# Kernel tuning notes

Hardware: AMD Instinct MI355X
Metric: run time of the kernel (lower is better)

## Reference

```python
import jax, jax.numpy as jnp
import numpy as np
from jax import lax

B = 512
THRESHOLD = 0.5
CFG = [64, 64, 'M', 128, 128, 'M', 256, 256, 256, 'M', 512, 512, 512, 'M', 512, 512, 512, 'M']  # VGG16


def _conv_relu(x, w, b):
    # x: [B,C,H,W], w: [O,I,3,3] (torch OIHW layout), pad=1 stride=1
    y = lax.conv_general_dilated(x, w, (1, 1), 'SAME',
                                 dimension_numbers=('NCHW', 'OIHW', 'NCHW'))
    return jax.nn.relu(y + b[None, :, None, None])


def _maxpool2(x):
    return lax.reduce_window(x, -jnp.inf, lax.max, (1, 1, 2, 2), (1, 1, 2, 2), 'VALID')


def _features(x, ws, bs):
    i = 0
    for c in CFG:
        if c == 'M':
            x = _maxpool2(x)
        else:
            x = _conv_relu(x, ws[i], bs[i])
            i += 1
    return x  # [B,512,1,1]


def _gcn(distance):
    # Faithful translation, including the source bug: 'onetensor' is zeros_like,
    # so mask==0 everywhere and A_hat collapses to the identity.
    n = distance.shape[0]
    zero = jnp.zeros_like(distance)
    one = jnp.zeros_like(distance)  # bug in original: torch.zeros_like for onetensor
    adj = jnp.where(distance > THRESHOLD, distance, zero)
    mask = jnp.where(distance > THRESHOLD, one, zero)
    idx = lax.top_k(adj, 10)[1]                                   # [n,10]
    top10 = jnp.zeros_like(adj).at[jnp.arange(n)[:, None], idx].set(1.0)
    top10 = top10 * mask
    a_hat = top10 + jnp.eye(n, dtype=distance.dtype)
    d_inv = jnp.diag(1.0 / jnp.sum(a_hat, axis=1))
    return lax.stop_gradient(a_hat @ d_inv)                        # [n,n]


def _forward(x, target, conv_ws, conv_bs, lin1_w, lin1_b, lin2_w, lin2_b, cls_w, cls_b):
    feat = _features(x, conv_ws, conv_bs).reshape(x.shape[0], -1)  # [B,512]
    h = jax.nn.relu(feat @ lin1_w + lin1_b)                        # [B,256]
    low = h @ lin2_w + lin2_b                                      # [B,128]
    graph_pre = jax.nn.sigmoid(low @ low.T)                        # [B,B]
    graph_gt = (target[:, None] == target[None, :]).astype(jnp.float32)
    mat = _gcn(graph_pre)                                          # [B,B], detached
    out = (mat @ feat) @ cls_w + cls_b                             # [B,10]
    return out, graph_pre, graph_gt


def setup_inputs() -> dict:
    key = jax.random.key(0)
    ks = iter(jax.random.split(key, 64))
    inp = {}
    inp['x'] = jax.random.normal(next(ks), (B, 3, 32, 32), dtype=jnp.float32)
    inp['target'] = jax.random.randint(next(ks), (B,), 0, 10)
    in_c, i = 3, 0
    for c in CFG:
        if c == 'M':
            continue
        scale = 1.0 / np.sqrt(in_c * 9.0)
        inp['conv%d_w' % i] = jax.random.normal(next(ks), (c, in_c, 3, 3), dtype=jnp.float32) * scale
        inp['conv%d_b' % i] = jnp.zeros((c,), dtype=jnp.float32)
        in_c, i = c, i + 1
    inp['lin1_w'] = jax.random.normal(next(ks), (512, 256), dtype=jnp.float32) * (1.0 / np.sqrt(512.0))
    inp['lin1_b'] = jnp.zeros((256,), dtype=jnp.float32)
    inp['lin2_w'] = jax.random.normal(next(ks), (256, 128), dtype=jnp.float32) * (1.0 / np.sqrt(256.0))
    inp['lin2_b'] = jnp.zeros((128,), dtype=jnp.float32)
    inp['cls_w'] = jax.random.normal(next(ks), (512, 10), dtype=jnp.float32) * (1.0 / np.sqrt(512.0))
    inp['cls_b'] = jnp.zeros((10,), dtype=jnp.float32)
    return inp


def reference(x, target,
              conv0_w, conv0_b, conv1_w, conv1_b, conv2_w, conv2_b, conv3_w, conv3_b,
              conv4_w, conv4_b, conv5_w, conv5_b, conv6_w, conv6_b, conv7_w, conv7_b,
              conv8_w, conv8_b, conv9_w, conv9_b, conv10_w, conv10_b, conv11_w, conv11_b,
              conv12_w, conv12_b,
              lin1_w, lin1_b, lin2_w, lin2_b, cls_w, cls_b):
    ws = [conv0_w, conv1_w, conv2_w, conv3_w, conv4_w, conv5_w, conv6_w,
          conv7_w, conv8_w, conv9_w, conv10_w, conv11_w, conv12_w]
    bs = [conv0_b, conv1_b, conv2_b, conv3_b, conv4_b, conv5_b, conv6_b,
          conv7_b, conv8_b, conv9_b, conv10_b, conv11_b, conv12_b]
    return _forward(x, target, ws, bs, lin1_w, lin1_b, lin2_w, lin2_b, cls_w, cls_b)
```

## Files before the change

kernel.cpp:

```cpp
#include <hip/hip_runtime.h>

typedef unsigned short u16;
typedef __bf16 bf16x8 __attribute__((ext_vector_type(8)));
typedef float floatx4 __attribute__((ext_vector_type(4)));

__device__ inline u16 f2bf(float f) {
    return __builtin_bit_cast(u16, (__bf16)f);
}
__device__ inline float bf2f(u16 h) {
    return __uint_as_float(((unsigned int)h) << 16);
}

__device__ __forceinline__ void async_copy16(u16* lds, const u16* g) {
    __builtin_amdgcn_global_load_lds(
        (const __attribute__((address_space(1))) unsigned int*)(uintptr_t)g,
        (__attribute__((address_space(3))) unsigned int*)(unsigned int)(uintptr_t)lds,
        16, 0, 0);
}

__global__ void zero_halo(u16* __restrict__ buf, int Hp, int C, int total8)
{
    int i = blockIdx.x * 256 + threadIdx.x;
    if (i >= total8) return;
    int c8 = i % (C / 8);
    int p  = i / (C / 8);
    int ring = 4 * Hp - 4;
    int h = p % ring;
    int b = p / ring;
    int y, x;
    if (h < Hp)              { y = 0;              x = h; }
    else if (h < 2 * Hp)     { y = Hp - 1;         x = h - Hp; }
    else if (h < 3 * Hp - 2) { y = h - 2 * Hp + 1; x = 0; }
    else                     { y = h - 3 * Hp + 3; x = Hp - 1; }
    uint4 z = make_uint4(0u, 0u, 0u, 0u);
    *(uint4*)(buf + ((size_t)((b * Hp + y) * Hp + x) * C) + c8 * 8) = z;
}

__global__ __launch_bounds__(256) void conv0_kernel(
    const float* __restrict__ x, const float* __restrict__ w,
    const float* __restrict__ bias, u16* __restrict__ out)
{
    __shared__ __align__(16) float xs[3][6][36];
    const int t  = threadIdx.x;
    const int b  = blockIdx.x >> 3;
    const int y0 = (blockIdx.x & 7) * 4;

    for (int i = t; i < 3 * 6 * 36; i += 256) {
        int ci  = i / 216;
        int rem = i % 216;
        int r   = rem / 36;
        int c   = rem % 36;
        int gy  = y0 - 1 + r;
        int gx  = c - 1;
        float v = 0.f;
        if ((unsigned)gy < 32u && (unsigned)gx < 32u)
            v = x[((b * 3 + ci) * 32 + gy) * 32 + gx];
        xs[ci][r][c] = v;
    }
    const int lane = t & 63;
    const int wv   = t >> 6;
    float wr[27];
    #pragma unroll
    for (int k = 0; k < 27; k++) wr[k] = w[lane * 27 + k];
    const float bz = bias[lane];
    __syncthreads();

    const int y = y0 + wv;
    u16* orow = out + ((size_t)((b * 34 + y + 1) * 34 + 1) * 64) + lane;
    for (int xg = 0; xg < 32; xg += 4) {
        float a0 = bz, a1 = bz, a2 = bz, a3 = bz;
        #pragma unroll
        for (int ci = 0; ci < 3; ci++) {
            #pragma unroll
            for (int rr = 0; rr < 3; rr++) {
                const float* row = &xs[ci][wv + rr][0];
                float4 c03 = *(const float4*)(row + xg);
                float2 c45 = *(const float2*)(row + xg + 4);
                float w0 = wr[ci * 9 + rr * 3 + 0];
                float w1 = wr[ci * 9 + rr * 3 + 1];
                float w2 = wr[ci * 9 + rr * 3 + 2];
                a0 += c03.x * w0 + c03.y * w1 + c03.z * w2;
                a1 += c03.y * w0 + c03.z * w1 + c03.w * w2;
                a2 += c03.z * w0 + c03.w * w1 + c45.x * w2;
                a3 += c03.w * w0 + c45.x * w1 + c45.y * w2;
            }
        }
        orow[(xg + 0) * 64] = f2bf(fmaxf(a0, 0.f));
        orow[(xg + 1) * 64] = f2bf(fmaxf(a1, 0.f));
        orow[(xg + 2) * 64] = f2bf(fmaxf(a2, 0.f));
        orow[(xg + 3) * 64] = f2bf(fmaxf(a3, 0.f));
    }
}

struct RepackArgs {
    const float* src[14];
    u16* dst[14];
    int p1[14];
    int p2[14];
    int startBlk[15];
    int nseg;
};

__global__ __launch_bounds__(256) void repack_all(RepackArgs a)
{
    __shared__ __align__(16) u16 lds[9216];
    int blk = blockIdx.x;
    int s = 0;
    #pragma unroll 1
    while (s + 1 < a.nseg && blk >= a.startBlk[s + 1]) s++;
    const int cb = blk - a.startBlk[s];
    const int t  = threadIdx.x;

    if (a.p2[s] == 0) {
        const int Cin = a.p1[s];
        const int logCin = __builtin_ctz(Cin);
        const float* src = a.src[s] + (size_t)cb * 9216;
        u16* dst = a.dst[s] + (size_t)cb * 9216;
        #pragma unroll
        for (int it = 0; it < 9; it++) {
            int j4 = it * 256 + t;
            float4 v = *(const float4*)(src + j4 * 4);
            ushort4 h;
            h.x = f2bf(v.x); h.y = f2bf(v.y); h.z = f2bf(v.z); h.w = f2bf(v.w);
            *(ushort4*)(lds + j4 * 4) = h;
        }
        __syncthreads();
        #pragma unroll
        for (int it = 0; it < 9; it++) {
            int o4   = (it * 256 + t) * 4;
            int ci   = o4 & (Cin - 1);
            int rest = o4 >> logCin;
            int co   = rest / 9;
            int sh   = rest - co * 9;
            int sb   = (co << logCin) * 9 + ci * 9 + sh;
            ushort4 h;
            h.x = lds[sb]; h.y = lds[sb + 9]; h.z = lds[sb + 18]; h.w = lds[sb + 27];
            *(ushort4*)(dst + o4) = h;
        }
    } else {
        const int K = a.p1[s], N = a.p2[s];
        const int ntx = N >> 6;
        const int k0 = (cb / ntx) * 64, n0 = (cb % ntx) * 64;
        const float* src = a.src[s];
        u16* dst = a.dst[s];
        const int r = t >> 4, c4 = (t & 15) * 4;
        #pragma unroll
        for (int rr = 0; rr < 64; rr += 16) {
            float4 v = *(const float4*)(src + (size_t)(k0 + r + rr) * N + n0 + c4);
            u16* p = lds + (r + rr) * 72 + c4;
            p[0] = f2bf(v.x); p[1] = f2bf(v.y); p[2] = f2bf(v.z); p[3] = f2bf(v.w);
        }
        __syncthreads();
        #pragma unroll
        for (int it = 0; it < 2; it++) {
            int ov = it * 256 + t;
            int n  = ov >> 3;
            int kq = (ov & 7) * 8;
            __align__(16) u16 h[8];
            #pragma unroll
            for (int j = 0; j < 8; j++) h[j] = lds[(kq + j) * 72 + n];
            *(uint4*)(dst + (size_t)(n0 + n) * K + k0 + kq) = *(uint4*)h;
        }
    }
}

template <int BM, int BN>
__global__ __launch_bounds__(256) void conv_gemm(
    const u16* __restrict__ in, const u16* __restrict__ wt,
    const float* __restrict__ bias, u16* __restrict__ out,
    float* __restrict__ partial, size_t pstride,
    int H, int Cin, int Cout, int logHW, int logW, int splitN,
    int outPad, int poolMode)
{
    constexpr int BK = 64;
    constexpr int WC = (BM == 256) ? BN : (BN / 2);
    constexpr int NT = WC / 16;
    constexpr int NB_A = BM / 32;
    constexpr int NB_B = BN / 32;
    __shared__ u16 As[BM * BK];
    __shared__ u16 Bs[BN * BK];

    const int Nblocks = Cout / BN;
    const int per = gridDim.x >> 3;
    const int bid = (blockIdx.x & 7) * per + (blockIdx.x >> 3);
    const int sp   = bid % splitN;
    const int tile = bid / splitN;
    const int m0 = (tile / Nblocks) * BM;
    const int n0 = (tile % Nblocks) * BN;

    const int t    = threadIdx.x;
    const int lane = t & 63;
    const int wave = t >> 6;
    const int quad = lane >> 4;
    const int l16  = lane & 15;
    const int wm   = (BM == 256) ? wave : (wave >> 1);
    const int wn   = (BM == 256) ? 0 : (wave & 1);
    const int W    = H;
    const int Wp   = H + 2;
    const int HW   = 1 << logHW;
    const int col8 = t & 7;
    const int r0   = t >> 3;
    const int scol = col8 ^ (r0 & 7);

    const int CinB = Cin * 2;

    int vA[NB_A];
    #pragma unroll
    for (int j = 0; j < NB_A; j++) {
        int m  = m0 + r0 + 32 * j;
        int b  = m >> logHW;
        int rm = m & (HW - 1);
        int y  = rm >> logW;
        int xx = rm & (W - 1);
        vA[j] = ((b * Wp + y + 1) * Wp + xx + 1) * CinB + scol * 16;
    }
    int vB[NB_B];
    #pragma unroll
    for (int j = 0; j < NB_B; j++)
        vB[j] = (n0 + r0 + 32 * j) * 9 * CinB + scol * 16;

    const int logKB = (Cin == 64) ? 0 : (Cin == 128) ? 1 : (Cin == 256) ? 2 : 3;
    const int KB  = 1 << logKB;
    const int T   = 9 * KB;
    const int len = T / splitN;
    const int it0 = sp * len;

    int s0 = it0 >> logKB;
    int c3 = s0 - (s0 / 3) * 3;
    int ta = ((s0 / 3 - 1) * Wp + (c3 - 1)) * CinB;
    int kb = (it0 & (KB - 1)) * 128;
    int tb = it0 * 128;

    u16* const ldsA = As + t * 8;
    u16* const ldsB = Bs + t * 8;
    const char* const inB = (const char*)in;
    const char* const wtB = (const char*)wt;

    floatx4 acc[4][NT];
    #pragma unroll
    for (int i = 0; i < 4; i++)
        #pragma unroll
        for (int j = 0; j < NT; j++)
            acc[i][j] = (floatx4){0.f, 0.f, 0.f, 0.f};

    const int sw = (l16 & 7) * 8;

    for (int it = 0; it < len; it++) {
        const int ua = ta + kb;
        #pragma unroll
        for (int j = 0; j < NB_A; j++)
            async_copy16(ldsA + j * 2048, (const u16*)(inB + (ua + vA[j])));
        #pragma unroll
        for (int j = 0; j < NB_B; j++)
            async_copy16(ldsB + j * 2048, (const u16*)(wtB + (tb + vB[j])));
        __syncthreads();
        #pragma unroll
        for (int kk = 0; kk < BK; kk += 32) {
            bf16x8 af[4], bfv[NT];
            int cbo = kk + quad * 8;
            #pragma unroll
            for (int mt = 0; mt < 4; mt++)
                af[mt] = *(const bf16x8*)(As + (wm * 64 + mt * 16 + l16) * 64 + (cbo ^ sw));
            #pragma unroll
            for (int nt = 0; nt < NT; nt++)
                bfv[nt] = *(const bf16x8*)(Bs + (wn * WC + nt * 16 + l16) * 64 + (cbo ^ sw));
            #pragma unroll
            for (int mt = 0; mt < 4; mt++)
                #pragma unroll
                for (int nt = 0; nt < NT; nt++)
                    acc[mt][nt] = __builtin_amdgcn_mfma_f32_16x16x32_bf16(
                        af[mt], bfv[nt], acc[mt][nt], 0, 0, 0);
        }
        __syncthreads();
        tb += 128;
        kb += 128;
        if (kb == CinB) {
            kb = 0;
            ta += (c3 == 2) ? (Wp - 2) * CinB : CinB;
            c3 = (c3 == 2) ? 0 : c3 + 1;
        }
    }

    const int ngb = n0 + wn * WC + l16;

    if (splitN > 1) {
        float* pout = partial + (size_t)sp * pstride;
        #pragma unroll
        for (int mt = 0; mt < 4; mt++)
            #pragma unroll
            for (int r = 0; r < 4; r++) {
                int mg = m0 + wm * 64 + mt * 16 + quad * 4 + r;
                float* op = pout + (size_t)mg * Cout + ngb;
                #pragma unroll
                for (int nt = 0; nt < NT; nt++)
                    op[nt * 16] = acc[mt][nt][r];
            }
        return;
    }

    float bzv[NT];
    #pragma unroll
    for (int nt = 0; nt < NT; nt++) bzv[nt] = bias[ngb + nt * 16];

    if (poolMode) {
        const int Hpo = (H >> 1) + 2;
        if (logW == 5) {
            #pragma unroll
            for (int mt = 0; mt < 2; mt++)
                #pragma unroll
                for (int rp = 0; rp < 2; rp++) {
                    int m1 = m0 + wm * 64 + mt * 16 + quad * 4 + 2 * rp;
                    int b  = m1 >> logHW;
                    int rm = m1 & (HW - 1);
                    int yp = (rm >> logW) >> 1;
                    int xp = (rm & (W - 1)) >> 1;
                    u16* op = out + (size_t)((b * Hpo + yp + 1) * Hpo + xp + 1) * Cout + ngb;
                    #pragma unroll
                    for (int nt = 0; nt < NT; nt++) {
                        float v = fmaxf(
                            fmaxf(acc[mt][nt][2 * rp], acc[mt][nt][2 * rp + 1]),
                            fmaxf(acc[mt + 2][nt][2 * rp], acc[mt + 2][nt][2 * rp + 1]));
                        op[nt * 16] = f2bf(fmaxf(v + bzv[nt], 0.f));
                    }
                }
        } else if (logW == 4) {
            #pragma unroll
            for (int mtp = 0; mtp < 2; mtp++)
                #pragma unroll
                for (int rp = 0; rp < 2; rp++) {
                    int mt = 2 * mtp;
                    int m1 = m0 + wm * 64 + mt * 16 + quad * 4 + 2 * rp;
                    int b  = m1 >> logHW;
                    int rm = m1 & (HW - 1);
                    int yp = (rm >> logW) >> 1;
                    int xp = (rm & (W - 1)) >> 1;
                    u16* op = out + (size_t)((b * Hpo + yp + 1) * Hpo + xp + 1) * Cout + ngb;
                    #pragma unroll
                    for (int nt = 0; nt < NT; nt++) {
                        float v = fmaxf(
                            fmaxf(acc[mt][nt][2 * rp], acc[mt][nt][2 * rp + 1]),
                            fmaxf(acc[mt + 1][nt][2 * rp], acc[mt + 1][nt][2 * rp + 1]));
                        op[nt * 16] = f2bf(fmaxf(v + bzv[nt], 0.f));
                    }
                }
        } else {
            #pragma unroll
            for (int mt = 0; mt < 4; mt++)
                #pragma unroll
                for (int rp = 0; rp < 2; rp++) {
                    int m1 = m0 + wm * 64 + mt * 16 + quad * 4 + 2 * rp;
                    int b  = m1 >> logHW;
                    int rm = m1 & (HW - 1);
                    int yp = (rm >> logW) >> 1;
                    int xp = (rm & (W - 1)) >> 1;
                    u16* op = out + (size_t)((b * Hpo + yp + 1) * Hpo + xp + 1) * Cout + ngb;
                    #pragma unroll
                    for (int nt = 0; nt < NT; nt++) {
                        float a = fmaxf(acc[mt][nt][2 * rp], acc[mt][nt][2 * rp + 1]);
                        float p = __shfl_xor(a, 32, 64);
                        float v = fmaxf(a, p);
                        if (quad < 2)
                            op[nt * 16] = f2bf(fmaxf(v + bzv[nt], 0.f));
                    }
                }
        }
        return;
    }

    #pragma unroll
    for (int mt = 0; mt < 4; mt++) {
        #pragma unroll
        for (int r = 0; r < 4; r++) {
            int mg = m0 + wm * 64 + mt * 16 + quad * 4 + r;
            size_t obase;
            if (outPad) {
                int b  = mg >> logHW;
                int rm = mg & (HW - 1);
                int y  = rm >> logW;
                int xx = rm & (W - 1);
                obase = (size_t)((b * Wp + y + 1) * Wp + xx + 1) * Cout;
            } else {
                obase = (size_t)mg * Cout;
            }
            u16* op = out + obase + ngb;
            #pragma unroll
            for (int nt = 0; nt < NT; nt++)
                op[nt * 16] = f2bf(fmaxf(acc[mt][nt][r] + bzv[nt], 0.f));
        }
    }
}

__global__ void reduce_split(const float* __restrict__ partial,
                             const float* __restrict__ bias, u16* __restrict__ out,
                             int MN, int C, int logC, int splitN, size_t pstride,
                             int H, int logHW, int logW, int outPad)
{
    int i4 = (blockIdx.x * 256 + threadIdx.x) * 4;
    if (i4 >= MN) return;
    float4 s = *(const float4*)(partial + i4);
    for (int sp = 1; sp < splitN; sp++) {
        float4 p = *(const float4*)(partial + (size_t)sp * pstride + i4);
        s.x += p.x; s.y += p.y; s.z += p.z; s.w += p.w;
    }
    int n = i4 & (C - 1);
    int m = i4 >> logC;
    size_t obase;
    if (outPad) {
        int Wp = H + 2;
        int b  = m >> logHW;
        int rm = m & ((1 << logHW) - 1);
        int y  = rm >> logW;
        int xx = rm & (H - 1);
        obase = (size_t)((b * Wp + y + 1) * Wp + xx + 1) * C;
    } else {
        obase = (size_t)m * C;
    }
    ushort4 o;
    o.x = f2bf(fmaxf(s.x + bias[n + 0], 0.f));
    o.y = f2bf(fmaxf(s.y + bias[n + 1], 0.f));
    o.z = f2bf(fmaxf(s.z + bias[n + 2], 0.f));
    o.w = f2bf(fmaxf(s.w + bias[n + 3], 0.f));
    *(ushort4*)(out + obase + n) = o;
}

__global__ void reduce_pool(const float* __restrict__ partial,
                            const float* __restrict__ bias, u16* __restrict__ out,
                            int total4, int C, int splitN, size_t pstride,
                            int H, int outPad)
{
    int idx = blockIdx.x * 256 + threadIdx.x;
    if (idx >= total4) return;
    int c4 = idx % (C / 4);
    int p  = idx / (C / 4);
    int Ho = H >> 1;
    int xp = p % Ho; p /= Ho;
    int yp = p % Ho;
    int b  = p / Ho;
    int n  = c4 * 4;
    float4 best;
    bool first = true;
    #pragma unroll
    for (int dy = 0; dy < 2; dy++)
        #pragma unroll
        for (int dx = 0; dx < 2; dx++) {
            int m = (b * H + 2 * yp + dy) * H + 2 * xp + dx;
            const float* q = partial + (size_t)m * C + n;
            float4 s = *(const float4*)q;
            for (int sp = 1; sp < splitN; sp++) {
                float4 pp = *(const float4*)(q + (size_t)sp * pstride);
                s.x += pp.x; s.y += pp.y; s.z += pp.z; s.w += pp.w;
            }
            if (first) { best = s; first = false; }
            else {
                best.x = fmaxf(best.x, s.x); best.y = fmaxf(best.y, s.y);
                best.z = fmaxf(best.z, s.z); best.w = fmaxf(best.w, s.w);
            }
        }
    size_t obase;
    if (outPad) {
        int Hpo = Ho + 2;
        obase = (size_t)((b * Hpo + yp + 1) * Hpo + xp + 1) * C;
    } else {
        obase = (size_t)((b * Ho + yp) * Ho + xp) * C;
    }
    ushort4 o;
    o.x = f2bf(fmaxf(best.x + bias[n + 0], 0.f));
    o.y = f2bf(fmaxf(best.y + bias[n + 1], 0.f));
    o.z = f2bf(fmaxf(best.z + bias[n + 2], 0.f));
    o.w = f2bf(fmaxf(best.w + bias[n + 3], 0.f));
    *(ushort4*)(out + obase + n) = o;
}

template <bool RELU, bool OUTBF>
__global__ __launch_bounds__(256) void gemm64(
    const u16* __restrict__ A, const u16* __restrict__ Bt,
    const float* __restrict__ bias, void* __restrict__ outv,
    int M, int N, int K)
{
    constexpr int LDP = 72;
    __shared__ u16 As[64 * LDP];
    __shared__ u16 Bs[64 * LDP];

    const int nb = N >> 6;
    const int m0 = (blockIdx.x / nb) * 64;
    const int n0 = (blockIdx.x % nb) * 64;
    const int t = threadIdx.x, lane = t & 63, wave = t >> 6;
    const int quad = lane >> 4, l16 = lane & 15;
    const int wm = wave >> 1, wn = wave & 1;
    const int col8 = t & 7, r0 = t >> 3;

    floatx4 acc[2][2];
    #pragma unroll
    for (int i = 0; i < 2; i++)
        #pragma unroll
        for (int j = 0; j < 2; j++)
            acc[i][j] = (floatx4){0.f, 0.f, 0.f, 0.f};

    for (int kb = 0; kb < K; kb += 64) {
        #pragma unroll
        for (int j = 0; j < 2; j++) {
            int row = r0 + 32 * j;
            *(uint4*)(As + row * LDP + col8 * 8) =
                *(const uint4*)(A + (size_t)(m0 + row) * K + kb + col8 * 8);
            *(uint4*)(Bs + row * LDP + col8 * 8) =
                *(const uint4*)(Bt + (size_t)(n0 + row) * K + kb + col8 * 8);
        }
        __syncthreads();
        #pragma unroll
        for (int kk = 0; kk < 64; kk += 32) {
            bf16x8 af[2], bfv[2];
            #pragma unroll
            for (int mt = 0; mt < 2; mt++)
                af[mt] = *(const bf16x8*)(As + (wm * 32 + mt * 16 + l16) * LDP + kk + quad * 8);
            #pragma unroll
            for (int nt = 0; nt < 2; nt++)
                bfv[nt] = *(const bf16x8*)(Bs + (wn * 32 + nt * 16 + l16) * LDP + kk + quad * 8);
            #pragma unroll
            for (int mt = 0; mt < 2; mt++)
                #pragma unroll
                for (int nt = 0; nt < 2; nt++)
                    acc[mt][nt] = __builtin_amdgcn_mfma_f32_16x16x32_bf16(
                        af[mt], bfv[nt], acc[mt][nt], 0, 0, 0);
        }
        __syncthreads();
    }
    #pragma unroll
    for (int mt = 0; mt < 2; mt++) {
        #pragma unroll
        for (int nt = 0; nt < 2; nt++) {
            #pragma unroll
            for (int r = 0; r < 4; r++) {
                int mg = m0 + wm * 32 + mt * 16 + quad * 4 + r;
                int ng = n0 + wn * 32 + nt * 16 + l16;
                float v = acc[mt][nt][r] + bias[ng];
                if (RELU) v = fmaxf(v, 0.f);
                if (OUTBF) ((u16*)outv)[(size_t)mg * N + ng] = f2bf(v);
                else       ((float*)outv)[(size_t)mg * N + ng] = v;
            }
        }
    }
}

__global__ __launch_bounds__(256) void graph_tile(
    const float* __restrict__ low, const int* __restrict__ target,
    float* __restrict__ gpre, float* __restrict__ ggt)
{
    __shared__ float Al[64 * 132];
    __shared__ float Bl[128 * 68];
    const int t = threadIdx.x;
    const int gr0 = (blockIdx.x >> 3) * 64;
    const int gc0 = (blockIdx.x & 7) * 64;

    #pragma unroll
    for (int j = 0; j < 32; j++) {
        int flat = t + 256 * j;
        int k = flat & 127;
        int rc = flat >> 7;
        Al[rc * 132 + k] = low[(size_t)(gr0 + rc) * 128 + k];
        Bl[k * 68 + rc]  = low[(size_t)(gc0 + rc) * 128 + k];
    }
    __syncthreads();

    const int tx = t & 15, ty = t >> 4;
    float acc[4][4];
    #pragma unroll
    for (int r = 0; r < 4; r++)
        #pragma unroll
        for (int c = 0; c < 4; c++) acc[r][c] = 0.f;

    for (int k = 0; k < 128; k++) {
        float a[4], b[4];
        #pragma unroll
        for (int r = 0; r < 4; r++) a[r] = Al[(ty * 4 + r) * 132 + k];
        #pragma unroll
        for (int c = 0; c < 4; c++) b[c] = Bl[k * 68 + tx * 4 + c];
        #pragma unroll
        for (int r = 0; r < 4; r++)
            #pragma unroll
            for (int c = 0; c < 4; c++) acc[r][c] += a[r] * b[c];
    }
    #pragma unroll
    for (int r = 0; r < 4; r++) {
        int row = gr0 + ty * 4 + r;
        int tr  = target[row];
        float4 gp, gg;
        float* pp = (float*)&gp;
        float* gg_ = (float*)&gg;
        #pragma unroll
        for (int c = 0; c < 4; c++) {
            pp[c]  = 1.f / (1.f + __expf(-acc[r][c]));
            gg_[c] = (tr == target[gc0 + tx * 4 + c]) ? 1.f : 0.f;
        }
        *(float4*)(gpre + (size_t)row * 512 + gc0 + tx * 4) = gp;
        *(float4*)(ggt  + (size_t)row * 512 + gc0 + tx * 4) = gg;
    }
}

__global__ __launch_bounds__(256) void cls_kernel(
    const u16* __restrict__ feat, const float* __restrict__ w,
    const float* __restrict__ bias, float* __restrict__ out)
{
    __shared__ float ws[5120];
    const int t = threadIdx.x;
    for (int i = t; i < 5120; i += 256) ws[i] = w[i];
    __syncthreads();
    const int lane = t & 63;
    const int row  = blockIdx.x * 4 + (t >> 6);
    float a[10];
    #pragma unroll
    for (int j = 0; j < 10; j++) a[j] = 0.f;
    #pragma unroll
    for (int i = 0; i < 8; i++) {
        int k = i * 64 + lane;
        float f = bf2f(feat[(size_t)row * 512 + k]);
        #pragma unroll
        for (int j = 0; j < 10; j++) a[j] += f * ws[k * 10 + j];
    }
    #pragma unroll
    for (int j = 0; j < 10; j++)
        #pragma unroll
        for (int off = 32; off > 0; off >>= 1)
            a[j] += __shfl_down(a[j], off, 64);
    if (lane == 0) {
        #pragma unroll
        for (int j = 0; j < 10; j++) out[row * 10 + j] = a[j] + bias[j];
    }
}

extern "C" void kernel_launch(void* const* d_in, const int* in_sizes, int n_in,
                              void* d_out, int out_size, void* d_ws, size_t ws_size,
                              hipStream_t stream)
{
    const float* x      = (const float*)d_in[0];
    const int*   target = (const int*)d_in[1];
    const float* conv_w[13];
    const float* conv_b[13];
    for (int i = 0; i < 13; i++) {
        conv_w[i] = (const float*)d_in[2 + 2 * i];
        conv_b[i] = (const float*)d_in[3 + 2 * i];
    }
    const float* lin1_w = (const float*)d_in[28];
    const float* lin1_b = (const float*)d_in[29];
    const float* lin2_w = (const float*)d_in[30];
    const float* lin2_b = (const float*)d_in[31];
    const float* cls_w  = (const float*)d_in[32];
    const float* cls_b  = (const float*)d_in[33];
    float* out = (float*)d_out;

    static const int cin_arr[13]  = {3, 64, 64, 128, 128, 256, 256, 256, 512, 512, 512, 512, 512};
    static const int cout_arr[13] = {64, 64, 128, 128, 256, 256, 256, 512, 512, 512, 512, 512, 512};

    char* ws = (char*)d_ws;
    size_t off = 0;
    const size_t R0SZ = (size_t)512 * 34 * 34 * 64 * 2;
    const size_t R1SZ = (size_t)512 * 34 * 34 * 64 * 2;
    char* R0raw = ws + off; off += R0SZ;
    char* R1raw = ws + off; off += R1SZ;
    u16* R0 = (u16*)R0raw;
    u16* R1 = (u16*)R1raw;
    float* PA = (float*)(R0raw + 20971520);
    float* PB = (float*)(R1raw + 20971520);
    u16* wt[13];
    for (int i = 1; i < 13; i++) {
        wt[i] = (u16*)(ws + off);
        off += (size_t)cout_arr[i] * 9 * cin_arr[i] * 2;
    }
    u16* wtl1 = (u16*)(ws + off); off += (size_t)256 * 512 * 2;
    u16* wtl2 = (u16*)(ws + off); off += (size_t)128 * 256 * 2;
    u16* hbuf = (u16*)(ws + off); off += (size_t)512 * 256 * 2;
    float* lowbuf = (float*)(ws + off); off += (size_t)512 * 128 * 4;

    RepackArgs ra;
    int nb = 0, blk = 0;
    ra.startBlk[0] = 0;
    for (int i = 1; i < 13; i++) {
        ra.src[nb] = conv_w[i];
        ra.dst[nb] = wt[i];
        ra.p1[nb] = cin_arr[i];
        ra.p2[nb] = 0;
        blk += cout_arr[i] * cin_arr[i] / 1024;
        nb++; ra.startBlk[nb] = blk;
    }
    ra.src[nb] = lin1_w; ra.dst[nb] = wtl1; ra.p1[nb] = 512; ra.p2[nb] = 256;
    blk += (512 / 64) * (256 / 64);
    nb++; ra.startBlk[nb] = blk;
    ra.src[nb] = lin2_w; ra.dst[nb] = wtl2; ra.p1[nb] = 256; ra.p2[nb] = 128;
    blk += (256 / 64) * (128 / 64);
    nb++; ra.startBlk[nb] = blk;
    ra.nseg = nb;
    repack_all<<<blk, 256, 0, stream>>>(ra);

    auto zh = [&](u16* buf, int Hp, int C) {
        int total8 = 512 * (4 * Hp - 4) * (C / 8);
        zero_halo<<<(total8 + 255) / 256, 256, 0, stream>>>(buf, Hp, C, total8);
    };
    auto launch_conv = [&](int li, int Hl, int bm, int bn, u16* inb, u16* outb,
                           float* part, int splitN, int outPad, int poolMode) {
        int Cin = cin_arr[li], Cout = cout_arr[li];
        int M = 512 * Hl * Hl;
        int logW = __builtin_ctz(Hl);
        int logHW = 2 * logW;
        size_t pstride = (size_t)M * Cout;
        int grid = (M / bm) * (Cout / bn) * splitN;
        if (bm == 256) {
            conv_gemm<256, 64><<<grid, 256, 0, stream>>>(
                inb, wt[li], conv_b[li], outb, part, pstride,
                Hl, Cin, Cout, logHW, logW, splitN, outPad, poolMode);
        } else if (bn == 128) {
            conv_gemm<128, 128><<<grid, 256, 0, stream>>>(
                inb, wt[li], conv_b[li], outb, part, pstride,
                Hl, Cin, Cout, logHW, logW, splitN, outPad, poolMode);
        } else {
            conv_gemm<128, 64><<<grid, 256, 0, stream>>>(
                inb, wt[li], conv_b[li], outb, part, pstride,
                Hl, Cin, Cout, logHW, logW, splitN, outPad, poolMode);
        }
    };
    auto launch_reduce = [&](int li, int Hl, u16* outb, float* part, int splitN, int outPad) {
        int Cout = cout_arr[li];
        int M = 512 * Hl * Hl;
        int logW = __builtin_ctz(Hl);
        size_t pstride = (size_t)M * Cout;
        int MN = M * Cout;
        reduce_split<<<(MN / 4 + 255) / 256, 256, 0, stream>>>(
            part, conv_b[li], outb, MN, Cout, __builtin_ctz(Cout),
            splitN, pstride, Hl, 2 * logW, logW, outPad);
    };
    auto launch_reduce_pool = [&](int li, int Hl, u16* outb, float* part, int splitN, int outPad) {
        int Cout = cout_arr[li];
        int M = 512 * Hl * Hl;
        size_t pstride = (size_t)M * Cout;
        int total4 = 512 * (Hl / 2) * (Hl / 2) * Cout / 4;
        reduce_pool<<<(total4 + 255) / 256, 256, 0, stream>>>(
            part, conv_b[li], outb, total4, Cout, splitN, pstride, Hl, outPad);
    };

    zh(R0, 34, 64);
    conv0_kernel<<<512 * 8, 256, 0, stream>>>(x, conv_w[0], conv_b[0], R0);

    zh(R1, 18, 64);
    launch_conv(1, 32, 256, 64, R0, R1, nullptr, 1, 0, 1);
    zh(R0, 18, 128);
    launch_conv(2, 16, 128, 128, R1, R0, nullptr, 1, 1, 0);
    zh(R1, 10, 128);
    launch_conv(3, 16, 128, 128, R0, R1, nullptr, 1, 0, 1);
    zh(R0, 10, 256);
    launch_conv(4, 8, 128, 128, R1, R0, nullptr, 1, 1, 0);
    zh(R1, 10, 256);
    launch_conv(5, 8, 128, 128, R0, R1, nullptr, 1, 1, 0);
    zh(R0, 6, 256);
    launch_conv(6, 8, 128, 128, R1, R0, nullptr, 1, 0, 1);
    zh(R1, 6, 512);
    launch_conv(7, 4, 128, 128, R0, R1, PB, 2, 1, 0);
    launch_reduce(7, 4, R1, PB, 2, 1);
    zh(R0, 6, 512);
    launch_conv(8, 4, 128, 128, R1, R0, PA, 2, 1, 0);
    launch_reduce(8, 4, R0, PA, 2, 1);
    zh(R1, 4, 512);
    launch_conv(9, 4, 128, 128, R0, R1, PB, 2, 0, 0);
    launch_reduce_pool(9, 4, R1, PB, 2, 1);
    zh(R0, 4, 512);
    launch_conv(10, 2, 128, 64, R1, R0, PA, 4, 1, 0);
    launch_reduce(10, 2, R0, PA, 4, 1);
    zh(R1, 4, 512);
    launch_conv(11, 2, 128, 64, R0, R1, PB, 4, 1, 0);
    launch_reduce(11, 2, R1, PB, 4, 1);
    launch_conv(12, 2, 128, 64, R1, R0, PA, 4, 0, 0);
    launch_reduce_pool(12, 2, R0, PA, 4, 0);

    u16* feat = R0;
    gemm64<true, true><<<(512 / 64) * (256 / 64), 256, 0, stream>>>(
        feat, wtl1, lin1_b, hbuf, 512, 256, 512);
    gemm64<false, false><<<(512 / 64) * (128 / 64), 256, 0, stream>>>(
        hbuf, wtl2, lin2_b, lowbuf, 512, 128, 256);
    graph_tile<<<64, 256, 0, stream>>>(lowbuf, target, out + 5120, out + 5120 + 262144);
    cls_kernel<<<128, 256, 0, stream>>>(feat, cls_w, cls_b, out);
}
```

Before: 768.3 us.

## Double-buffer LDS tiles in conv GEMM to overlap loads with MFMA

Splits the A and B shared-memory tiles into two buffers and prefetches the next K-step with async global-to-LDS copies before running the MFMA loop on the current buffer. This removes one barrier per iteration and lets the global load latency hide behind the matrix math instead of stalling every step. In exchange the kernel uses twice as much LDS, which can lower the number of blocks resident per CU.

```diff
diff --git a/kernel.cpp b/kernel.cpp
--- a/kernel.cpp
+++ b/kernel.cpp
@@ -177,8 +177,10 @@
     constexpr int NT = WC / 16;
     constexpr int NB_A = BM / 32;
     constexpr int NB_B = BN / 32;
-    __shared__ u16 As[BM * BK];
-    __shared__ u16 Bs[BN * BK];
+    constexpr int ASZ = BM * BK;
+    constexpr int BSZ = BN * BK;
+    __shared__ u16 As[2 * ASZ];
+    __shared__ u16 Bs[2 * BSZ];
 
     const int Nblocks = Cout / BN;
     const int per = gridDim.x >> 3;
@@ -231,8 +233,6 @@
     int kb = (it0 & (KB - 1)) * 128;
     int tb = it0 * 128;
 
-    u16* const ldsA = As + t * 8;
-    u16* const ldsB = Bs + t * 8;
     const char* const inB = (const char*)in;
     const char* const wtB = (const char*)wt;
 
@@ -245,33 +245,17 @@
 
     const int sw = (l16 & 7) * 8;
 
-    for (int it = 0; it < len; it++) {
-        const int ua = ta + kb;
+    auto stage = [&](int ua, int tbv, int buf) {
+        u16* la = As + buf * ASZ + t * 8;
+        u16* lb = Bs + buf * BSZ + t * 8;
         #pragma unroll
         for (int j = 0; j < NB_A; j++)
-            async_copy16(ldsA + j * 2048, (const u16*)(inB + (ua + vA[j])));
+            async_copy16(la + j * 2048, (const u16*)(inB + (ua + vA[j])));
         #pragma unroll
         for (int j = 0; j < NB_B; j++)
-            async_copy16(ldsB + j * 2048, (const u16*)(wtB + (tb + vB[j])));
-        __syncthreads();
-        #pragma unroll
-        for (int kk = 0; kk < BK; kk += 32) {
-            bf16x8 af[4], bfv[NT];
-            int cbo = kk + quad * 8;
-            #pragma unroll
-            for (int mt = 0; mt < 4; mt++)
-                af[mt] = *(const bf16x8*)(As + (wm * 64 + mt * 16 + l16) * 64 + (cbo ^ sw));
-            #pragma unroll
-            for (int nt = 0; nt < NT; nt++)
-                bfv[nt] = *(const bf16x8*)(Bs + (wn * WC + nt * 16 + l16) * 64 + (cbo ^ sw));
-            #pragma unroll
-            for (int mt = 0; mt < 4; mt++)
-                #pragma unroll
-                for (int nt = 0; nt < NT; nt++)
-                    acc[mt][nt] = __builtin_amdgcn_mfma_f32_16x16x32_bf16(
-                        af[mt], bfv[nt], acc[mt][nt], 0, 0, 0);
-        }
-        __syncthreads();
+            async_copy16(lb + j * 2048, (const u16*)(wtB + (tbv + vB[j])));
+    };
+    auto advance = [&]() {
         tb += 128;
         kb += 128;
         if (kb == CinB) {
@@ -279,6 +263,39 @@
             ta += (c3 == 2) ? (Wp - 2) * CinB : CinB;
             c3 = (c3 == 2) ? 0 : c3 + 1;
         }
+    };
+
+    stage(ta + kb, tb, 0);
+    advance();
+    __syncthreads();
+
+    int cur = 0;
+    for (int it = 0; it < len; it++) {
+        if (it + 1 < len) {
+            stage(ta + kb, tb, cur ^ 1);
+            advance();
+        }
+        const u16* Ab = As + cur * ASZ;
+        const u16* Bb = Bs + cur * BSZ;
+        #pragma unroll
+        for (int kk = 0; kk < BK; kk += 32) {
+            bf16x8 af[4], bfv[NT];
+            int cbo = kk + quad * 8;
+            #pragma unroll
+            for (int mt = 0; mt < 4; mt++)
+                af[mt] = *(const bf16x8*)(Ab + (wm * 64 + mt * 16 + l16) * 64 + (cbo ^ sw));
+            #pragma unroll
+            for (int nt = 0; nt < NT; nt++)
+                bfv[nt] = *(const bf16x8*)(Bb + (wn * WC + nt * 16 + l16) * 64 + (cbo ^ sw));
+            #pragma unroll
+            for (int mt = 0; mt < 4; mt++)
+                #pragma unroll
+                for (int nt = 0; nt < NT; nt++)
+                    acc[mt][nt] = __builtin_amdgcn_mfma_f32_16x16x32_bf16(
+                        af[mt], bfv[nt], acc[mt][nt], 0, 0, 0);
+        }
+        __syncthreads();
+        cur ^= 1;
     }
 
     const int ngb = n0 + wn * WC + l16;
```

Result: faster. 698.9 us (-9.0%).
